# Kernel tuning notes

Measured on AMD Instinct MI355X. Metric: run time of the kernel, lower is better.

## Reference

```python
import jax, jax.numpy as jnp
import numpy as np

BATCH = 8
NUM_CLASSES = 80
COF_DIM = 128  # num_basic_masks(32) * sub_region_x(2) * sub_region_y(2)
STRIDES = (8, 16, 32)
SIZES = ((100, 152), (50, 76), (25, 38))
IMG_H, IMG_W = 800, 1216
PRE_NMS_THRESH = 0.05
PRE_NMS_TOP_N = 1000
NMS_THRESH = 0.6
POST_NMS_TOP_N = 100
THRESH_WITH_CTR = False
CLASS_OFFSET = float(max(IMG_H, IMG_W) + 1)  # batched_nms class-offset trick


def _make_locations(h, w, stride):
    xs = jnp.arange(w, dtype=jnp.float32) * stride + stride // 2
    ys = jnp.arange(h, dtype=jnp.float32) * stride + stride // 2
    Y, X = jnp.meshgrid(ys, xs, indexing='ij')
    return jnp.stack([X.reshape(-1), Y.reshape(-1)], axis=-1)  # [HW,2] (x,y)


def setup_inputs() -> dict:
    key = jax.random.key(0)
    inp = {}
    for i, ((h, w), s) in enumerate(zip(SIZES, STRIDES)):
        k1, k2, k3, k4, key = jax.random.split(key, 5)
        inp[f'locations{i}'] = _make_locations(h, w, s)
        # shift logits down so the pre_nms threshold actually prunes some candidates
        inp[f'logits{i}'] = jax.random.normal(k1, (BATCH, NUM_CLASSES, h, w), jnp.float32) - 2.0
        inp[f'reg{i}'] = jax.random.uniform(k2, (BATCH, 4, h, w), jnp.float32, minval=0.5, maxval=8.0)
        inp[f'ctr{i}'] = jax.random.normal(k3, (BATCH, 1, h, w), jnp.float32)
        inp[f'cofs{i}'] = jax.random.normal(k4, (BATCH, COF_DIM, h, w), jnp.float32)
    return inp


def _level(locs, logits, reg, ctr, cofs, stride):
    # faithful port of forward_for_single_feature_map, fixed-size (padded) version
    N, C, H, W = logits.shape
    HW = H * W
    K = PRE_NMS_TOP_N
    scores = jax.nn.sigmoid(logits).transpose(0, 2, 3, 1).reshape(N, HW, C)
    reg = reg.transpose(0, 2, 3, 1).reshape(N, HW, 4) * stride
    ctr = jax.nn.sigmoid(ctr.reshape(N, HW))
    cofs = cofs.transpose(0, 2, 3, 1).reshape(N, HW, -1)
    if THRESH_WITH_CTR:
        scores = scores * ctr[:, :, None]
    cand = scores > PRE_NMS_THRESH
    if not THRESH_WITH_CTR:
        scores = scores * ctr[:, :, None]
    flat = jnp.where(cand, scores, -1.0).reshape(N, HW * C)
    n_cand = jnp.minimum(cand.reshape(N, -1).sum(-1), K)  # per-image pre_nms_top_n clamp
    vals, idx = jax.lax.top_k(flat, K)
    valid = jnp.arange(K)[None, :] < n_cand[:, None]
    loc_idx = idx // C
    cls = idx % C
    pl = locs[loc_idx]                                        # [N,K,2]
    pr = jnp.take_along_axis(reg, loc_idx[..., None], axis=1)  # [N,K,4]
    pc = jnp.take_along_axis(cofs, loc_idx[..., None], axis=1) # [N,K,COF_DIM]
    x1 = jnp.clip(pl[..., 0] - pr[..., 0], 0.0, IMG_W)
    y1 = jnp.clip(pl[..., 1] - pr[..., 1], 0.0, IMG_H)
    x2 = jnp.clip(pl[..., 0] + pr[..., 2], 0.0, IMG_W)
    y2 = jnp.clip(pl[..., 1] + pr[..., 3], 0.0, IMG_H)
    boxes = jnp.stack([x1, y1, x2, y2], axis=-1)
    return boxes, vals, cls, pc, valid


def _pairwise_iou(b):
    area = (b[:, 2] - b[:, 0]) * (b[:, 3] - b[:, 1])
    lt = jnp.maximum(b[:, None, :2], b[None, :, :2])
    rb = jnp.minimum(b[:, None, 2:], b[None, :, 2:])
    wh = jnp.clip(rb - lt, 0.0, None)
    inter = wh[..., 0] * wh[..., 1]
    return inter / (area[:, None] + area[None, :] - inter + 1e-9)


def _nms_single(boxes, scores, classes, cofs, valid):
    # ml_nms / batched_nms: class-offset boxes, greedy suppression, keep top post_nms_top_n
    K = boxes.shape[0]
    s = jnp.where(valid, scores, -1.0)
    order = jnp.argsort(-s)
    b = boxes[order]
    sv = s[order]
    c = classes[order]
    pc = cofs[order]
    v = valid[order]
    ob = b + (c.astype(b.dtype) * CLASS_OFFSET)[:, None]
    sup = _pairwise_iou(ob) > NMS_THRESH
    idxs = jnp.arange(K)
    def body(i, keep):
        return keep & ~(keep[i] & sup[i] & (idxs > i))
    keep = jax.lax.fori_loop(0, K, body, v)
    final = jnp.where(keep, sv, -1.0)
    _, topi = jax.lax.top_k(final, POST_NMS_TOP_N)
    kv = keep[topi]
    out_boxes = jnp.where(kv[:, None], b[topi], 0.0)
    # FCOS/SipMask reports sqrt(cls_score * ctrness)
    out_scores = jnp.where(kv, jnp.sqrt(jnp.maximum(sv[topi], 1e-12)), 0.0)
    out_cls = jnp.where(kv, c[topi], -1)
    out_cofs = jnp.where(kv[:, None], pc[topi], 0.0)
    return out_boxes, out_scores, out_cls, out_cofs, kv


def reference(locations0, logits0, reg0, ctr0, cofs0,
              locations1, logits1, reg1, ctr1, cofs1,
              locations2, logits2, reg2, ctr2, cofs2):
    levels = [(locations0, logits0, reg0, ctr0, cofs0),
              (locations1, logits1, reg1, ctr1, cofs1),
              (locations2, logits2, reg2, ctr2, cofs2)]
    outs = [_level(*lv, s) for lv, s in zip(levels, STRIDES)]
    boxes = jnp.concatenate([o[0] for o in outs], axis=1)
    scores = jnp.concatenate([o[1] for o in outs], axis=1)
    classes = jnp.concatenate([o[2] for o in outs], axis=1)
    cofs = jnp.concatenate([o[3] for o in outs], axis=1)
    valid = jnp.concatenate([o[4] for o in outs], axis=1)
    return jax.vmap(_nms_single)(boxes, scores, classes, cofs, valid)
```

## Files before the change

kernel.cpp:

```cpp
#include <hip/hip_runtime.h>

typedef unsigned int u32;
typedef unsigned long long u64;

#define NCLS 80
#define NIMG 8
#define PRE_K 1000
#define POST_K 100
#define PBUF_N 2048

__device__ __forceinline__ int HWof(int l){ return l==0?15200:(l==1?3800:950); }
__device__ __forceinline__ float STRof(int l){ return l==0?8.f:(l==1?16.f:32.f); }
__device__ __forceinline__ u32 CAPof(int l){ return l==0?65536u:32768u; }
__device__ __forceinline__ u32 POFFof(int l){ return l==0?0u:(l==1?65536u:98304u); }

struct Ptrs {
  const float* logits[3];
  const float* reg[3];
  const float* ctr[3];
  const float* cofs[3];
  const float* locs[3];
};

#define NB0 149
#define NB1 38
#define NBALL 197

#define OFF_HIST1 0u
#define OFF_PCNT  49152u
#define OFF_THR   49248u
#define OFF_MCNT  50016u
#define OFF_KEEP  50048u
#define ZERO_BYTES 53120u
#define OFF_POOL  53248u
#define OFF_SORT  8441856u
#define OFF_CLS   8638464u
#define OFF_MERG  8736768u

__device__ __forceinline__ float sigmoidf(float x){ return 1.0f/(1.0f+expf(-x)); }

template<int LVL, bool REFILL>
__device__ __forceinline__ void pass_body(int tile, int img, const Ptrs& p,
                                          u32* pcnt, const u32* thr, u64* pool,
                                          u64* pbuf, u32* shctl, u32* lh, u32* hist1){
  constexpr int HW   = LVL==0?15200:(LVL==1?3800:950);
  constexpr int NE   = 80*HW;
  constexpr int NF4  = NE/4;
  const u32 CAP = CAPof(LVL);
  const int pair = img*3 + LVL;
  const size_t poff = (size_t)img*131072u + POFFof(LVL);
  const u32 tbin = REFILL ? thr[pair*8+0] : (LVL==0?501u:(LVL==1?500u:496u));
  const float4* plane = (const float4*)(p.logits[LVL] + (size_t)img*NE);
  const float* cptr = p.ctr[LVL] + (size_t)img*HW;
  if (!REFILL){ for (int b=threadIdx.x;b<512;b+=256) lh[b]=0; }
  if (threadIdx.x==0) shctl[0]=0;
  __syncthreads();
  #pragma unroll
  for (int k=0;k<8;++k){
    int f4 = tile*2048 + k*256 + (int)threadIdx.x;
    if (f4 < NF4){
      float4 v = plane[f4];
      int e0 = f4*4;
      int cls0 = e0 / HW;
      int loc0 = e0 - cls0*HW;
      float ss[4];
      if (LVL==2){
        #pragma unroll
        for (int j=0;j<4;++j){ int e=e0+j; int c=e/HW; ss[j]=sigmoidf(cptr[e-c*HW]); }
      } else {
        float4 c4 = *(const float4*)(cptr + loc0);
        ss[0]=sigmoidf(c4.x); ss[1]=sigmoidf(c4.y); ss[2]=sigmoidf(c4.z); ss[3]=sigmoidf(c4.w);
      }
      float vv[4] = {v.x,v.y,v.z,v.w};
      #pragma unroll
      for (int j=0;j<4;++j){
        float sl = sigmoidf(vv[j]);
        if (sl > 0.05f){
          u32 bits = __float_as_uint(sl * ss[j]);
          if (!REFILL) atomicAdd(&lh[bits>>21], 1u);
          if ((bits>>21) >= tbin){
            int e = e0 + j, cls, loc;
            if (LVL==2){ cls=e/HW; loc=e-cls*HW; } else { cls=cls0; loc=loc0+j; }
            u64 key = ((u64)bits<<32) | (u64)(0xFFFFFFFFu - (u32)(loc*NCLS + cls));
            u32 id = atomicAdd(&shctl[0], 1u);
            if (id < (u32)PBUF_N) pbuf[id] = key;
            else { u32 g = atomicAdd(&pcnt[pair],1u); if (g<CAP) pool[poff+g]=key; }
          }
        }
      }
    }
  }
  __syncthreads();
  u32 m = shctl[0]; if (m > (u32)PBUF_N) m = PBUF_N;
  if (threadIdx.x==0 && m) shctl[2] = atomicAdd(&pcnt[pair], m);
  __syncthreads();
  for (u32 i=threadIdx.x; i<m; i+=256){
    u32 d = shctl[2] + i;
    if (d < CAP) pool[poff+d] = pbuf[i];
  }
  if (!REFILL){
    for (int b=threadIdx.x;b<512;b+=256){ u32 c=lh[b]; if (c) atomicAdd(&hist1[pair*512+b], c); }
  }
}

__global__ __launch_bounds__(256)
void fused_pass(Ptrs p, u32* pcnt, u64* pool, u32* hist1){
  __shared__ u64 pbuf[PBUF_N];
  __shared__ u32 shctl[4];
  __shared__ u32 lh[512];
  const int bx=(int)blockIdx.x, img=(int)blockIdx.y;
  if (bx<NB0)          pass_body<0,false>(bx,        img,p,pcnt,nullptr,pool,pbuf,shctl,lh,hist1);
  else if (bx<NB0+NB1) pass_body<1,false>(bx-NB0,    img,p,pcnt,nullptr,pool,pbuf,shctl,lh,hist1);
  else                 pass_body<2,false>(bx-NB0-NB1,img,p,pcnt,nullptr,pool,pbuf,shctl,lh,hist1);
}

__global__ __launch_bounds__(256)
void select_kernel(const u32* hist1, u32* pcnt, u32* thr, const u64* pool){
  const int pair=(int)blockIdx.x, lvl=pair%3, img=pair/3;
  __shared__ u32 h[512];
  __shared__ u32 h2[2048];
  __shared__ u32 seg[256], exc[256];
  __shared__ u32 sB1, sCnt, sTot;
  const int t = (int)threadIdx.x;
  u32 b0 = hist1[pair*512 + (511-2*t)];
  u32 b1 = hist1[pair*512 + (511-(2*t+1))];
  h[511-2*t]=b0; h[511-(2*t+1)]=b1;
  seg[t]=b0+b1;
  __syncthreads();
  if (t==0){ u32 run=0; for(int i=0;i<256;++i){ exc[i]=run; run+=seg[i]; } sTot=run; }
  __syncthreads();
  const u32 kk = min(sTot, (u32)PRE_K);
  if (t==0){
    thr[pair*8+3]=kk;
    if (kk==0){ thr[pair*8+2]=0xFFFFFFFFu; thr[pair*8+4]=1u; }
  }
  if (kk==0) return;
  u32 cum = exc[t];
  #pragma unroll
  for (int q=0;q<2;++q){
    int bin = 511-(2*t+q); u32 c=h[bin];
    if (c && cum<kk && cum+c>=kk){ sB1=(u32)bin; sCnt=cum; }
    cum+=c;
  }
  __syncthreads();
  const u32 B1=sB1, cntAb=sCnt;
  const u32 tbin = lvl==0?501u:(lvl==1?500u:496u);
  const u32 pc = pcnt[pair];
  const bool ok = (pc <= CAPof(lvl)) && (B1 >= tbin);
  if (t==0){
    thr[pair*8+0]=B1; thr[pair*8+1]=cntAb; thr[pair*8+4]=ok?1u:0u;
    if (!ok) pcnt[pair]=0;
  }
  if (!ok) return;
  for (int b=t;b<2048;b+=256) h2[b]=0;
  __syncthreads();
  const size_t poff = (size_t)img*131072u + POFFof(lvl);
  for (u32 i=t;i<pc;i+=256){
    u64 key = pool[poff+i];
    if ((u32)(key>>53)==B1) atomicAdd(&h2[(u32)(key>>42)&0x7FFu],1u);
  }
  __syncthreads();
  const u32 KK2 = kk - cntAb;
  u32 part=0;
  #pragma unroll
  for (int q=0;q<8;++q) part += h2[2047-(t*8+q)];
  seg[t]=part;
  __syncthreads();
  if (t==0){ u32 run=0; for(int i=0;i<256;++i){ exc[i]=run; run+=seg[i]; } }
  __syncthreads();
  cum = exc[t];
  #pragma unroll
  for (int q=0;q<8;++q){
    int bin=2047-(t*8+q); u32 c=h2[bin];
    if (c && cum<KK2 && cum+c>=KK2) thr[pair*8+2]=(B1<<11)|(u32)bin;
    cum+=c;
  }
}

__global__ __launch_bounds__(256)
void refill_pass(Ptrs p, u32* pcnt, const u32* thr, u64* pool){
  const int bx=(int)blockIdx.x, img=(int)blockIdx.y;
  const int lvl = bx<NB0?0:(bx<NB0+NB1?1:2);
  if (thr[(img*3+lvl)*8+4]) return;
  __shared__ u64 pbuf[PBUF_N];
  __shared__ u32 shctl[4];
  if (lvl==0)      pass_body<0,true>(bx,        img,p,pcnt,thr,pool,pbuf,shctl,nullptr,nullptr);
  else if (lvl==1) pass_body<1,true>(bx-NB0,    img,p,pcnt,thr,pool,pbuf,shctl,nullptr,nullptr);
  else             pass_body<2,true>(bx-NB0-NB1,img,p,pcnt,thr,pool,pbuf,shctl,nullptr,nullptr);
}

__global__ __launch_bounds__(1024)
void sort_pool(u32* thr, const u32* pcnt, const u64* pool, u64* sorted){
  const int pair=(int)blockIdx.x, lvl=pair%3, img=pair/3;
  __shared__ u64 a[2048];
  __shared__ u32 cnt;
  __shared__ u32 h2[2048], seg[256], exc[256];
  __shared__ u32 sT22;
  const int tid=(int)threadIdx.x;
  const u32 kk = thr[pair*8+3];
  const size_t poff = (size_t)img*131072u + POFFof(lvl);
  const u32 pc = min(pcnt[pair], CAPof(lvl));
  const u32 ok = thr[pair*8+4];
  if (tid==0) sT22 = thr[pair*8+2];
  __syncthreads();
  if (!ok && kk){
    const u32 B1 = thr[pair*8+0];
    const u32 KK2 = kk - thr[pair*8+1];
    for (int b=tid;b<2048;b+=1024) h2[b]=0;
    __syncthreads();
    for (u32 i=tid;i<pc;i+=1024){
      u64 key = pool[poff+i];
      if ((u32)(key>>53)==B1) atomicAdd(&h2[(u32)(key>>42)&0x7FFu],1u);
    }
    __syncthreads();
    if (tid<256){
      u32 part=0;
      #pragma unroll
      for (int q=0;q<8;++q) part += h2[2047-(tid*8+q)];
      seg[tid]=part;
    }
    __syncthreads();
    if (tid==0){ u32 run=0; for(int i=0;i<256;++i){ exc[i]=run; run+=seg[i]; } }
    __syncthreads();
    if (tid<256){
      u32 cum = exc[tid];
      #pragma unroll
      for (int q=0;q<8;++q){
        int bin=2047-(tid*8+q); u32 c=h2[bin];
        if (c && cum<KK2 && cum+c>=KK2) sT22=(B1<<11)|(u32)bin;
        cum+=c;
      }
    }
    __syncthreads();
  }
  const u32 T22 = sT22;
  for (int i=tid;i<2048;i+=1024) a[i]=0ull;
  if (tid==0) cnt=0;
  __syncthreads();
  for (u32 i=tid;i<pc;i+=1024){
    u64 k = pool[poff+i];
    if ((u32)(k>>42) >= T22){
      u32 id = atomicAdd(&cnt,1u);
      if (id < 2048u) a[id]=k;
    }
  }
  __syncthreads();
  const u32 n = min(cnt, 2048u);
  for (int k=2;k<=2048;k<<=1){
    for (int j=k>>1;j>0;j>>=1){
      for (int t=tid;t<2048;t+=1024){
        int ix = t ^ j;
        if (ix > t){
          u64 x=a[t], y=a[ix];
          bool up = ((t & k)==0);
          if (up ? (x<y) : (x>y)){ a[t]=y; a[ix]=x; }
        }
      }
      __syncthreads();
    }
  }
  u32 m = kk < n ? kk : n;
  for (u32 r=tid;r<m;r+=1024) sorted[(size_t)pair*1024+r]=a[r];
  if (tid==0) thr[pair*8+3]=m;
}

__global__ void merge_kernel(Ptrs p, const u32* thr, const u64* sorted,
                             float* merged, float* clsarr, u32* mcnt){
#pragma clang fp contract(off)
  const int img = blockIdx.x;
  __shared__ u64 mk[3][1024];
  __shared__ int n[3];
  if (threadIdx.x < 3) n[threadIdx.x] = (int)thr[(img*3+threadIdx.x)*8+3];
  __syncthreads();
  const int n0=n[0], n1=n[1], n2=n[2];
  for (int idx=threadIdx.x; idx<3*1024; idx+=blockDim.x){
    int l = idx>>10, r = idx&1023;
    if (r < n[l]){
      u64 key = sorted[(size_t)(img*3+l)*1024 + r];
      mk[l][r] = (key & 0xFFFFFFFF00000000ull) |
                 (u64)(0xFFFFFFFFu - (u32)(l*PRE_K + r));
    }
  }
  __syncthreads();
  const int T = n0+n1+n2;
  if (threadIdx.x==0) mcnt[img] = (u32)T;
  for (int t=threadIdx.x; t<T; t+=blockDim.x){
    int l, r;
    if (t < n0){ l=0; r=t; }
    else if (t < n0+n1){ l=1; r=t-n0; }
    else { l=2; r=t-n0-n1; }
    u64 x = mk[l][r];
    int pos = r;
    #pragma unroll
    for (int o=0;o<3;++o) if (o!=l){
      int lo=0, hi=n[o];
      while (lo<hi){ int m=(lo+hi)>>1; if (mk[o][m] > x) lo=m+1; else hi=m; }
      pos += lo;
    }
    u64 key = sorted[(size_t)(img*3+l)*1024 + r];
    u32 flat = 0xFFFFFFFFu - (u32)(key & 0xFFFFFFFFull);
    float score = __uint_as_float((u32)(key>>32));
    int HW = HWof(l);
    int loc = (int)(flat / (u32)NCLS);
    int cls = (int)(flat - (u32)loc*NCLS);
    float lx = p.locs[l][2*loc], ly = p.locs[l][2*loc+1];
    float st = STRof(l);
    const float* rg = p.reg[l] + (size_t)img*4*HW + loc;
    float r0 = rg[0]*st, r1 = rg[HW]*st, r2 = rg[2*(size_t)HW]*st, r3 = rg[3*(size_t)HW]*st;
    float x1 = fminf(fmaxf(lx - r0, 0.f), 1216.f);
    float y1 = fminf(fmaxf(ly - r1, 0.f),  800.f);
    float x2 = fminf(fmaxf(lx + r2, 0.f), 1216.f);
    float y2 = fminf(fmaxf(ly + r3, 0.f),  800.f);
    float* out = merged + (size_t)(img*3072 + pos)*8;
    out[0]=x1; out[1]=y1; out[2]=x2; out[3]=y2;
    out[4]=score; out[5]=(float)cls; out[6]=(float)l; out[7]=(float)loc;
    clsarr[img*3072 + pos] = (float)cls;
  }
}

__global__ __launch_bounds__(64)
void nms_class(const float* merged_all, const float* clsarr, const u32* mcnt, u64* gkeep){
#pragma clang fp contract(off)
  const int c = (int)blockIdx.x, img = (int)blockIdx.y;
  const float* merged = merged_all + (size_t)img*3072*8;
  const float* carr = clsarr + (size_t)img*3072;
  const int T = (int)mcnt[img];
  const int lane = (int)threadIdx.x;
  __shared__ unsigned short mlist[3072];
  __shared__ float4 kbox[1024];

  float fv[48];
  #pragma unroll
  for (int w=0; w<48; ++w){
    int j = w*64 + lane;
    fv[w] = (j < T) ? carr[j] : -1.0f;
  }
  int base = 0;
  const u64 lanemask = (lane==0) ? 0ull : ((~0ull) >> (64-lane));
  #pragma unroll
  for (int w=0; w<48; ++w){
    bool mem = ((int)fv[w] == c);
    u64 word = __ballot(mem);
    if (mem){
      int rank = base + (int)__popcll(word & lanemask);
      mlist[rank] = (unsigned short)(w*64 + lane);
    }
    base += (int)__popcll(word);
  }
  const int n = base;
  if (n == 0) return;
  __syncthreads();

  const float off = (float)c * 1217.0f;
  int kc = 0;
  for (int t0 = 0; t0 < n; t0 += 64){
    int r = t0 + lane;
    bool valid = (r < n);
    float4 bx = make_float4(0.f,0.f,0.f,0.f);
    int gj = 0;
    if (valid){
      gj = (int)mlist[r];
      const float* rec = merged + (size_t)gj*8;
      bx = make_float4(rec[0]+off, rec[1]+off, rec[2]+off, rec[3]+off);
    }
    float ax = (bx.z-bx.x)*(bx.w-bx.y);
    bool alive_l = valid;
    for (int q=0; q<kc; ++q){
      float4 bq = kbox[q];
      float aq = (bq.z-bq.x)*(bq.w-bq.y);
      float ltx=fmaxf(bq.x,bx.x), lty=fmaxf(bq.y,bx.y);
      float rbx=fminf(bq.z,bx.z), rby=fminf(bq.w,bx.w);
      float wx=fmaxf(rbx-ltx,0.f), wy=fmaxf(rby-lty,0.f);
      float inter=wx*wy;
      float denom=aq+ax; denom=denom-inter; denom=denom+1e-9f;
      if (alive_l && (inter/denom > 0.6f)) alive_l=false;
    }
    u64 alive = __ballot(alive_l);
    while (alive){
      int i = __ffsll((unsigned long long)alive) - 1;
      float bix=__shfl(bx.x,i), biy=__shfl(bx.y,i), biz=__shfl(bx.z,i), biw=__shfl(bx.w,i);
      int gi = __shfl(gj, i);
      if (lane==0){
        atomicOr((unsigned long long*)&gkeep[img*48 + (gi>>6)], 1ull<<(gi&63));
        if (kc < 1024) kbox[kc] = make_float4(bix,biy,biz,biw);
      }
      kc++;
      float ai=(biz-bix)*(biw-biy);
      float ltx=fmaxf(bix,bx.x), lty=fmaxf(biy,bx.y);
      float rbx=fminf(biz,bx.z), rby=fminf(biw,bx.w);
      float wx=fmaxf(rbx-ltx,0.f), wy=fmaxf(rby-lty,0.f);
      float inter=wx*wy;
      float denom=ai+ax; denom=denom-inter; denom=denom+1e-9f;
      bool supp = alive_l && (inter/denom > 0.6f);
      u64 killm = __ballot(supp);
      alive &= ~killm;
      alive &= ~(1ull<<i);
      alive_l = alive_l && !supp;
    }
    __syncthreads();
  }
}

__global__ __launch_bounds__(128)
void emit_kernel(Ptrs p, const float* merged_all, const u64* gkeep, float* out){
  const int r = (int)blockIdx.x, img = (int)blockIdx.y;
  const int tid = (int)threadIdx.x;
  __shared__ int s_i, s_kept;
  if (tid < 64){
    u64 word = (tid < 48) ? gkeep[img*48 + tid] : 0ull;
    int c = (int)__popcll(word);
    int inc = c;
    #pragma unroll
    for (int d=1; d<64; d<<=1){
      int y = __shfl_up(inc, d);
      if (tid >= d) inc += y;
    }
    int excl = inc - c;
    int total = __shfl(inc, 63);
    int kept = total < POST_K ? total : POST_K;
    if (tid==0){ s_kept = kept; s_i = -1; }
    bool sel = (tid<48) && (r < kept) && (excl <= r) && (r < excl + c);
    if (sel){
      u64 w = word; int need = r - excl;
      for (int q=0;q<need;++q) w &= w-1ull;
      s_i = (tid<<6) + (int)__ffsll((unsigned long long)w) - 1;
    }
  }
  __syncthreads();
  const int i = s_i; const int kept = s_kept;
  const bool has = (r < kept) && (i >= 0);
  const float* rec = merged_all + (size_t)img*3072*8 + (size_t)(has?i:0)*8;
  float* obx = out;
  float* osc = out + 3200;
  float* ocl = out + 4000;
  float* ocf = out + 4800;
  float* okv = out + 107200;
  if (tid==0) osc[img*POST_K+r] = has ? sqrtf(fmaxf(rec[4], 1e-12f)) : 0.f;
  if (tid==1) ocl[img*POST_K+r] = has ? rec[5] : -1.0f;
  if (tid==2) okv[img*POST_K+r] = has ? 1.0f : 0.f;
  if (tid>=4 && tid<8) obx[(img*POST_K+r)*4 + (tid-4)] = has ? rec[tid-4] : 0.f;
  float v = 0.f;
  if (has){
    int l = (int)rec[6]; int loc = (int)rec[7];
    int HW = HWof(l);
    v = p.cofs[l][((size_t)img*128 + tid)*HW + loc];
  }
  ocf[(img*POST_K + r)*128 + tid] = v;
}

extern "C" void kernel_launch(void* const* d_in, const int* in_sizes, int n_in,
                              void* d_out, int out_size, void* d_ws, size_t ws_size,
                              hipStream_t stream){
  Ptrs p;
  for (int l=0; l<3; ++l){
    p.locs[l]   = (const float*)d_in[5*l+0];
    p.logits[l] = (const float*)d_in[5*l+1];
    p.reg[l]    = (const float*)d_in[5*l+2];
    p.ctr[l]    = (const float*)d_in[5*l+3];
    p.cofs[l]   = (const float*)d_in[5*l+4];
  }
  char* ws = (char*)d_ws;
  u32* hist1  = (u32*)(ws + OFF_HIST1);
  u32* pcnt   = (u32*)(ws + OFF_PCNT);
  u32* thr    = (u32*)(ws + OFF_THR);
  u32* mcnt   = (u32*)(ws + OFF_MCNT);
  u64* gkeep  = (u64*)(ws + OFF_KEEP);
  u64* pool   = (u64*)(ws + OFF_POOL);
  u64* sorted = (u64*)(ws + OFF_SORT);
  float* clsarr = (float*)(ws + OFF_CLS);
  float* merged = (float*)(ws + OFF_MERG);

  hipMemsetAsync(ws, 0, ZERO_BYTES, stream);
  fused_pass<<<dim3(NBALL,8), 256, 0, stream>>>(p, pcnt, pool, hist1);
  select_kernel<<<24, 256, 0, stream>>>(hist1, pcnt, thr, pool);
  refill_pass<<<dim3(NBALL,8), 256, 0, stream>>>(p, pcnt, thr, pool);
  sort_pool<<<24, 1024, 0, stream>>>(thr, pcnt, pool, sorted);
  merge_kernel<<<8, 1024, 0, stream>>>(p, thr, sorted, merged, clsarr, mcnt);
  nms_class<<<dim3(NCLS,8), 64, 0, stream>>>(merged, clsarr, mcnt, gkeep);
  emit_kernel<<<dim3(POST_K,8), 128, 0, stream>>>(p, merged, gkeep, (float*)d_out);
}
```

Before: 172.1 us.

## Drop global histogram pass; merge select, refill and sort into one kernel

```diff
diff --git a/kernel.cpp b/kernel.cpp
--- a/kernel.cpp
+++ b/kernel.cpp
@@ -26,35 +26,35 @@
 #define NB1 38
 #define NBALL 197
 
-#define OFF_HIST1 0u
-#define OFF_PCNT  49152u
-#define OFF_THR   49248u
-#define OFF_MCNT  50016u
-#define OFF_KEEP  50048u
-#define ZERO_BYTES 53120u
-#define OFF_POOL  53248u
-#define OFF_SORT  8441856u
-#define OFF_CLS   8638464u
-#define OFF_MERG  8736768u
+#define OFF_PCNT  0u
+#define OFF_CAND  128u
+#define OFF_MCNT  256u
+#define OFF_KEEP  320u
+#define ZERO_BYTES 3392u
+#define OFF_THR   3392u
+#define OFF_POOL  4224u
+#define OFF_SORT  8392832u
+#define OFF_CLS   8589440u
+#define OFF_MERG  8687744u
 
 __device__ __forceinline__ float sigmoidf(float x){ return 1.0f/(1.0f+expf(-x)); }
 
-template<int LVL, bool REFILL>
-__device__ __forceinline__ void pass_body(int tile, int img, const Ptrs& p,
-                                          u32* pcnt, const u32* thr, u64* pool,
-                                          u64* pbuf, u32* shctl, u32* lh, u32* hist1){
+template<int LVL>
+__device__ __forceinline__ void collect_body(int tile, int img, const Ptrs& p,
+                                             u32* cand, u32* pcnt, u64* pool,
+                                             u64* pbuf, u32* shctl){
   constexpr int HW   = LVL==0?15200:(LVL==1?3800:950);
   constexpr int NE   = 80*HW;
   constexpr int NF4  = NE/4;
   const u32 CAP = CAPof(LVL);
   const int pair = img*3 + LVL;
   const size_t poff = (size_t)img*131072u + POFFof(LVL);
-  const u32 tbin = REFILL ? thr[pair*8+0] : (LVL==0?501u:(LVL==1?500u:496u));
+  const u32 tbin = (LVL==0?501u:(LVL==1?500u:496u));
   const float4* plane = (const float4*)(p.logits[LVL] + (size_t)img*NE);
   const float* cptr = p.ctr[LVL] + (size_t)img*HW;
-  if (!REFILL){ for (int b=threadIdx.x;b<512;b+=256) lh[b]=0; }
-  if (threadIdx.x==0) shctl[0]=0;
-  __syncthreads();
+  if (threadIdx.x==0){ shctl[0]=0; shctl[1]=0; }
+  __syncthreads();
+  u32 mc = 0;
   #pragma unroll
   for (int k=0;k<8;++k){
     int f4 = tile*2048 + k*256 + (int)threadIdx.x;
@@ -76,8 +76,8 @@
       for (int j=0;j<4;++j){
         float sl = sigmoidf(vv[j]);
         if (sl > 0.05f){
+          mc++;
           u32 bits = __float_as_uint(sl * ss[j]);
-          if (!REFILL) atomicAdd(&lh[bits>>21], 1u);
           if ((bits>>21) >= tbin){
             int e = e0 + j, cls, loc;
             if (LVL==2){ cls=e/HW; loc=e-cls*HW; } else { cls=cls0; loc=loc0+j; }
@@ -90,162 +90,171 @@
       }
     }
   }
+  if (mc) atomicAdd(&shctl[1], mc);
   __syncthreads();
   u32 m = shctl[0]; if (m > (u32)PBUF_N) m = PBUF_N;
-  if (threadIdx.x==0 && m) shctl[2] = atomicAdd(&pcnt[pair], m);
+  if (threadIdx.x==0){
+    if (m) shctl[2] = atomicAdd(&pcnt[pair], m);
+    if (shctl[1]) atomicAdd(&cand[pair], shctl[1]);
+  }
   __syncthreads();
   for (u32 i=threadIdx.x; i<m; i+=256){
     u32 d = shctl[2] + i;
     if (d < CAP) pool[poff+d] = pbuf[i];
   }
-  if (!REFILL){
-    for (int b=threadIdx.x;b<512;b+=256){ u32 c=lh[b]; if (c) atomicAdd(&hist1[pair*512+b], c); }
-  }
 }
 
 __global__ __launch_bounds__(256)
-void fused_pass(Ptrs p, u32* pcnt, u64* pool, u32* hist1){
+void fused_pass(Ptrs p, u32* cand, u32* pcnt, u64* pool){
   __shared__ u64 pbuf[PBUF_N];
   __shared__ u32 shctl[4];
-  __shared__ u32 lh[512];
   const int bx=(int)blockIdx.x, img=(int)blockIdx.y;
-  if (bx<NB0)          pass_body<0,false>(bx,        img,p,pcnt,nullptr,pool,pbuf,shctl,lh,hist1);
-  else if (bx<NB0+NB1) pass_body<1,false>(bx-NB0,    img,p,pcnt,nullptr,pool,pbuf,shctl,lh,hist1);
-  else                 pass_body<2,false>(bx-NB0-NB1,img,p,pcnt,nullptr,pool,pbuf,shctl,lh,hist1);
-}
-
-__global__ __launch_bounds__(256)
-void select_kernel(const u32* hist1, u32* pcnt, u32* thr, const u64* pool){
+  if (bx<NB0)          collect_body<0>(bx,        img,p,cand,pcnt,pool,pbuf,shctl);
+  else if (bx<NB0+NB1) collect_body<1>(bx-NB0,    img,p,cand,pcnt,pool,pbuf,shctl);
+  else                 collect_body<2>(bx-NB0-NB1,img,p,cand,pcnt,pool,pbuf,shctl);
+}
+
+template<int LVL>
+__device__ __forceinline__ void slow_hist(const Ptrs& p, int img, u32* h){
+  constexpr int HW = LVL==0?15200:(LVL==1?3800:950);
+  constexpr int NE = 80*HW, NF4 = NE/4;
+  const float4* plane = (const float4*)(p.logits[LVL] + (size_t)img*NE);
+  const float* cptr = p.ctr[LVL] + (size_t)img*HW;
+  for (int f4=(int)threadIdx.x; f4<NF4; f4+=1024){
+    float4 v = plane[f4];
+    int e0=f4*4;
+    float vv[4]={v.x,v.y,v.z,v.w};
+    #pragma unroll
+    for (int j=0;j<4;++j){
+      float sl=sigmoidf(vv[j]);
+      if (sl>0.05f){
+        int e=e0+j; int c=e/HW; int loc=e-c*HW;
+        u32 bits=__float_as_uint(sl*sigmoidf(cptr[loc]));
+        atomicAdd(&h[bits>>21],1u);
+      }
+    }
+  }
+}
+template<int LVL>
+__device__ __forceinline__ void slow_refill(const Ptrs& p, int img, u32 B1,
+                                            u64* pool, size_t poff, u32* cnt){
+  constexpr int HW = LVL==0?15200:(LVL==1?3800:950);
+  constexpr int NE = 80*HW, NF4 = NE/4;
+  const u32 CAP = CAPof(LVL);
+  const float4* plane = (const float4*)(p.logits[LVL] + (size_t)img*NE);
+  const float* cptr = p.ctr[LVL] + (size_t)img*HW;
+  for (int f4=(int)threadIdx.x; f4<NF4; f4+=1024){
+    float4 v = plane[f4];
+    int e0=f4*4;
+    float vv[4]={v.x,v.y,v.z,v.w};
+    #pragma unroll
+    for (int j=0;j<4;++j){
+      float sl=sigmoidf(vv[j]);
+      if (sl>0.05f){
+        int e=e0+j; int c=e/HW; int loc=e-c*HW;
+        u32 bits=__float_as_uint(sl*sigmoidf(cptr[loc]));
+        if ((bits>>21) >= B1){
+          u32 id = atomicAdd(cnt,1u);
+          if (id<CAP) pool[poff+id] = ((u64)bits<<32) |
+                        (u64)(0xFFFFFFFFu - (u32)(loc*NCLS + c));
+        }
+      }
+    }
+  }
+}
+
+__global__ __launch_bounds__(1024)
+void selsort(Ptrs p, const u32* cand, const u32* pcnt, u32* thr,
+             u64* pool, u64* sorted){
   const int pair=(int)blockIdx.x, lvl=pair%3, img=pair/3;
+  const int tid=(int)threadIdx.x;
+  __shared__ u64 a[2048];
   __shared__ u32 h[512];
   __shared__ u32 h2[2048];
   __shared__ u32 seg[256], exc[256];
-  __shared__ u32 sB1, sCnt, sTot;
-  const int t = (int)threadIdx.x;
-  u32 b0 = hist1[pair*512 + (511-2*t)];
-  u32 b1 = hist1[pair*512 + (511-(2*t+1))];
-  h[511-2*t]=b0; h[511-(2*t+1)]=b1;
-  seg[t]=b0+b1;
-  __syncthreads();
-  if (t==0){ u32 run=0; for(int i=0;i<256;++i){ exc[i]=run; run+=seg[i]; } sTot=run; }
-  __syncthreads();
-  const u32 kk = min(sTot, (u32)PRE_K);
-  if (t==0){
-    thr[pair*8+3]=kk;
-    if (kk==0){ thr[pair*8+2]=0xFFFFFFFFu; thr[pair*8+4]=1u; }
-  }
-  if (kk==0) return;
-  u32 cum = exc[t];
-  #pragma unroll
-  for (int q=0;q<2;++q){
-    int bin = 511-(2*t+q); u32 c=h[bin];
-    if (c && cum<kk && cum+c>=kk){ sB1=(u32)bin; sCnt=cum; }
-    cum+=c;
+  __shared__ u32 sB1, sCnt, sT22, sgc, scnt;
+  const size_t poff = (size_t)img*131072u + POFFof(lvl);
+  const u32 CAP = CAPof(lvl);
+  const u32 kk = min(cand[pair], (u32)PRE_K);
+  if (kk==0){ if (tid==0) thr[pair*8+3]=0u; return; }
+  const u32 pcRaw = pcnt[pair];
+  const bool ok = (pcRaw <= CAP) && (pcRaw >= kk);
+  u32 pc = min(pcRaw, CAP);
+
+  for (int b=tid;b<512;b+=1024) h[b]=0;
+  __syncthreads();
+  if (ok){
+    for (u32 i=tid;i<pc;i+=1024) atomicAdd(&h[(u32)(pool[poff+i]>>53)],1u);
+  } else {
+    if (lvl==0)      slow_hist<0>(p,img,h);
+    else if (lvl==1) slow_hist<1>(p,img,h);
+    else             slow_hist<2>(p,img,h);
+  }
+  __syncthreads();
+  if (tid<256) seg[tid] = h[511-2*tid] + h[511-(2*tid+1)];
+  __syncthreads();
+  if (tid==0){ u32 run=0; for(int i=0;i<256;++i){ exc[i]=run; run+=seg[i]; } }
+  __syncthreads();
+  if (tid<256){
+    u32 cum=exc[tid];
+    #pragma unroll
+    for (int q=0;q<2;++q){
+      int bin=511-(2*tid+q); u32 c=h[bin];
+      if (c && cum<kk && cum+c>=kk){ sB1=(u32)bin; sCnt=cum; }
+      cum+=c;
+    }
   }
   __syncthreads();
   const u32 B1=sB1, cntAb=sCnt;
-  const u32 tbin = lvl==0?501u:(lvl==1?500u:496u);
-  const u32 pc = pcnt[pair];
-  const bool ok = (pc <= CAPof(lvl)) && (B1 >= tbin);
-  if (t==0){
-    thr[pair*8+0]=B1; thr[pair*8+1]=cntAb; thr[pair*8+4]=ok?1u:0u;
-    if (!ok) pcnt[pair]=0;
-  }
-  if (!ok) return;
-  for (int b=t;b<2048;b+=256) h2[b]=0;
-  __syncthreads();
-  const size_t poff = (size_t)img*131072u + POFFof(lvl);
-  for (u32 i=t;i<pc;i+=256){
-    u64 key = pool[poff+i];
+  if (!ok){
+    if (tid==0) sgc=0;
+    __syncthreads();
+    if (lvl==0)      slow_refill<0>(p,img,B1,pool,poff,&sgc);
+    else if (lvl==1) slow_refill<1>(p,img,B1,pool,poff,&sgc);
+    else             slow_refill<2>(p,img,B1,pool,poff,&sgc);
+    __syncthreads();
+    pc = min(sgc, CAP);
+  }
+  for (int b=tid;b<2048;b+=1024) h2[b]=0;
+  __syncthreads();
+  for (u32 i=tid;i<pc;i+=1024){
+    u64 key=pool[poff+i];
     if ((u32)(key>>53)==B1) atomicAdd(&h2[(u32)(key>>42)&0x7FFu],1u);
   }
   __syncthreads();
   const u32 KK2 = kk - cntAb;
-  u32 part=0;
-  #pragma unroll
-  for (int q=0;q<8;++q) part += h2[2047-(t*8+q)];
-  seg[t]=part;
-  __syncthreads();
-  if (t==0){ u32 run=0; for(int i=0;i<256;++i){ exc[i]=run; run+=seg[i]; } }
-  __syncthreads();
-  cum = exc[t];
-  #pragma unroll
-  for (int q=0;q<8;++q){
-    int bin=2047-(t*8+q); u32 c=h2[bin];
-    if (c && cum<KK2 && cum+c>=KK2) thr[pair*8+2]=(B1<<11)|(u32)bin;
-    cum+=c;
-  }
-}
-
-__global__ __launch_bounds__(256)
-void refill_pass(Ptrs p, u32* pcnt, const u32* thr, u64* pool){
-  const int bx=(int)blockIdx.x, img=(int)blockIdx.y;
-  const int lvl = bx<NB0?0:(bx<NB0+NB1?1:2);
-  if (thr[(img*3+lvl)*8+4]) return;
-  __shared__ u64 pbuf[PBUF_N];
-  __shared__ u32 shctl[4];
-  if (lvl==0)      pass_body<0,true>(bx,        img,p,pcnt,thr,pool,pbuf,shctl,nullptr,nullptr);
-  else if (lvl==1) pass_body<1,true>(bx-NB0,    img,p,pcnt,thr,pool,pbuf,shctl,nullptr,nullptr);
-  else             pass_body<2,true>(bx-NB0-NB1,img,p,pcnt,thr,pool,pbuf,shctl,nullptr,nullptr);
-}
-
-__global__ __launch_bounds__(1024)
-void sort_pool(u32* thr, const u32* pcnt, const u64* pool, u64* sorted){
-  const int pair=(int)blockIdx.x, lvl=pair%3, img=pair/3;
-  __shared__ u64 a[2048];
-  __shared__ u32 cnt;
-  __shared__ u32 h2[2048], seg[256], exc[256];
-  __shared__ u32 sT22;
-  const int tid=(int)threadIdx.x;
-  const u32 kk = thr[pair*8+3];
-  const size_t poff = (size_t)img*131072u + POFFof(lvl);
-  const u32 pc = min(pcnt[pair], CAPof(lvl));
-  const u32 ok = thr[pair*8+4];
-  if (tid==0) sT22 = thr[pair*8+2];
-  __syncthreads();
-  if (!ok && kk){
-    const u32 B1 = thr[pair*8+0];
-    const u32 KK2 = kk - thr[pair*8+1];
-    for (int b=tid;b<2048;b+=1024) h2[b]=0;
-    __syncthreads();
-    for (u32 i=tid;i<pc;i+=1024){
-      u64 key = pool[poff+i];
-      if ((u32)(key>>53)==B1) atomicAdd(&h2[(u32)(key>>42)&0x7FFu],1u);
-    }
-    __syncthreads();
-    if (tid<256){
-      u32 part=0;
-      #pragma unroll
-      for (int q=0;q<8;++q) part += h2[2047-(tid*8+q)];
-      seg[tid]=part;
-    }
-    __syncthreads();
-    if (tid==0){ u32 run=0; for(int i=0;i<256;++i){ exc[i]=run; run+=seg[i]; } }
-    __syncthreads();
-    if (tid<256){
-      u32 cum = exc[tid];
-      #pragma unroll
-      for (int q=0;q<8;++q){
-        int bin=2047-(tid*8+q); u32 c=h2[bin];
-        if (c && cum<KK2 && cum+c>=KK2) sT22=(B1<<11)|(u32)bin;
-        cum+=c;
-      }
-    }
-    __syncthreads();
-  }
-  const u32 T22 = sT22;
+  if (tid<256){
+    u32 part=0;
+    #pragma unroll
+    for (int q=0;q<8;++q) part += h2[2047-(tid*8+q)];
+    seg[tid]=part;
+  }
+  __syncthreads();
+  if (tid==0){ u32 run=0; for(int i=0;i<256;++i){ exc[i]=run; run+=seg[i]; } }
+  __syncthreads();
+  if (tid<256){
+    u32 cum=exc[tid];
+    #pragma unroll
+    for (int q=0;q<8;++q){
+      int bin=2047-(tid*8+q); u32 c=h2[bin];
+      if (c && cum<KK2 && cum+c>=KK2) sT22=(B1<<11)|(u32)bin;
+      cum+=c;
+    }
+  }
+  __syncthreads();
+  const u32 T22=sT22;
   for (int i=tid;i<2048;i+=1024) a[i]=0ull;
-  if (tid==0) cnt=0;
+  if (tid==0) scnt=0;
   __syncthreads();
   for (u32 i=tid;i<pc;i+=1024){
     u64 k = pool[poff+i];
     if ((u32)(k>>42) >= T22){
-      u32 id = atomicAdd(&cnt,1u);
+      u32 id = atomicAdd(&scnt,1u);
       if (id < 2048u) a[id]=k;
     }
   }
   __syncthreads();
-  const u32 n = min(cnt, 2048u);
+  const u32 n = min(scnt, 2048u);
   for (int k=2;k<=2048;k<<=1){
     for (int j=k>>1;j>0;j>>=1){
       for (int t=tid;t<2048;t+=1024){
@@ -460,21 +469,19 @@
     p.cofs[l]   = (const float*)d_in[5*l+4];
   }
   char* ws = (char*)d_ws;
-  u32* hist1  = (u32*)(ws + OFF_HIST1);
   u32* pcnt   = (u32*)(ws + OFF_PCNT);
-  u32* thr    = (u32*)(ws + OFF_THR);
+  u32* cand   = (u32*)(ws + OFF_CAND);
   u32* mcnt   = (u32*)(ws + OFF_MCNT);
   u64* gkeep  = (u64*)(ws + OFF_KEEP);
+  u32* thr    = (u32*)(ws + OFF_THR);
   u64* pool   = (u64*)(ws + OFF_POOL);
   u64* sorted = (u64*)(ws + OFF_SORT);
   float* clsarr = (float*)(ws + OFF_CLS);
   float* merged = (float*)(ws + OFF_MERG);
 
   hipMemsetAsync(ws, 0, ZERO_BYTES, stream);
-  fused_pass<<<dim3(NBALL,8), 256, 0, stream>>>(p, pcnt, pool, hist1);
-  select_kernel<<<24, 256, 0, stream>>>(hist1, pcnt, thr, pool);
-  refill_pass<<<dim3(NBALL,8), 256, 0, stream>>>(p, pcnt, thr, pool);
-  sort_pool<<<24, 1024, 0, stream>>>(thr, pcnt, pool, sorted);
+  fused_pass<<<dim3(NBALL,8), 256, 0, stream>>>(p, cand, pcnt, pool);
+  selsort<<<24, 1024, 0, stream>>>(p, cand, pcnt, thr, pool, sorted);
   merge_kernel<<<8, 1024, 0, stream>>>(p, thr, sorted, merged, clsarr, mcnt);
   nms_class<<<dim3(NCLS,8), 64, 0, stream>>>(merged, clsarr, mcnt, gkeep);
   emit_kernel<<<dim3(POST_K,8), 128, 0, stream>>>(p, merged, gkeep, (float*)d_out);
```

Result: faster. 163.0 us, median of 2 (-5.3%).
